# Kernel tuning notes

Measured on AMD Instinct MI355X. Metric: run time of the kernel, lower is better.

The kernel has to match this reference:

```python
import jax, jax.numpy as jnp
import numpy as np

N_HEADS = 16


def _rope_table(seq_len, head_dim):
    # Matches RotaryPositionalEmbedding: emb = cat(sin(pos*inv_freq), cos(pos*inv_freq))
    inv_freq = 1.0 / (10000.0 ** (jnp.arange(0, head_dim, 2, dtype=jnp.float32) / head_dim))
    sinusoid = jnp.arange(seq_len, dtype=jnp.float32)[:, None] * inv_freq[None, :]  # [S, hd/2]
    return jnp.sin(sinusoid), jnp.cos(sinusoid)


def _apply_rope(q, k, seq_len, head_dim):
    # Faithful to the torch code, which slices emb[:, :hd/2] (== sin) and calls it 'cos',
    # and emb[:, hd/2:] (== cos) and calls it 'sin'. We keep that exact math.
    sin_tab, cos_tab = _rope_table(seq_len, head_dim)
    c = sin_tab[None, None]  # named 'cos' in torch code, actually sin values
    s = cos_tab[None, None]  # named 'sin' in torch code, actually cos values
    half = head_dim // 2
    def rot(x):
        x1, x2 = x[..., :half], x[..., half:]
        return jnp.concatenate([x1 * c - x2 * s, x2 * c + x1 * s], axis=-1)
    return rot(q), rot(k)


def setup_inputs() -> dict:
    key = jax.random.key(0)
    ks = jax.random.split(key, 9)
    B, S, D = 4, 2048, 1024
    sc = 1.0 / np.sqrt(D)
    return {
        'hidden_states': jax.random.normal(ks[0], (B, S, D), jnp.float32),
        'Wq': jax.random.normal(ks[1], (D, D), jnp.float32) * sc,
        'bq': jax.random.normal(ks[2], (D,), jnp.float32) * 0.01,
        'Wk': jax.random.normal(ks[3], (D, D), jnp.float32) * sc,
        'bk': jax.random.normal(ks[4], (D,), jnp.float32) * 0.01,
        'Wv': jax.random.normal(ks[5], (D, D), jnp.float32) * sc,
        'bv': jax.random.normal(ks[6], (D,), jnp.float32) * 0.01,
        'Wo': jax.random.normal(ks[7], (D, D), jnp.float32) * sc,
        'bo': jax.random.normal(ks[8], (D,), jnp.float32) * 0.01,
    }


def reference(hidden_states, Wq, bq, Wk, bk, Wv, bv, Wo, bo):
    B, S, D = hidden_states.shape
    H = N_HEADS
    hd = D // H

    def proj(W, b):
        y = jnp.einsum('bsd,ed->bse', hidden_states, W) + b  # nn.Linear: x @ W.T + b
        return y.reshape(B, S, H, hd).transpose(0, 2, 1, 3)   # [B,H,S,hd]

    q = proj(Wq, bq)
    k = proj(Wk, bk)
    v = proj(Wv, bv)
    q, k = _apply_rope(q, k, S, hd)

    scale = 1.0 / np.sqrt(hd)
    scores = jnp.einsum('bhqd,bhkd->bhqk', q, k) * scale  # [B,H,S,S]
    attn = jax.nn.softmax(scores, axis=-1)
    ctx = jnp.einsum('bhqk,bhkd->bhqd', attn, v)          # [B,H,S,hd]
    ctx = ctx.transpose(0, 2, 1, 3).reshape(B, S, D)
    return jnp.einsum('bsd,ed->bse', ctx, Wo) + bo
```

## Files before the change

### kernel.cpp

```cpp
#include <hip/hip_runtime.h>
#include <math.h>

#define SEQ 2048
#define DMODEL 1024
#define NH 16
#define HD 64
#define BH 64
#define MROWS 8192
#define QKV_U16 8388608
#define LOG2E 1.4426950408889634f

typedef __attribute__((ext_vector_type(8))) _Float16 half8;
typedef __attribute__((ext_vector_type(4))) _Float16 half4;
typedef __attribute__((ext_vector_type(2))) __fp16 fp16v2;
typedef __attribute__((ext_vector_type(8))) short short8;
typedef __attribute__((ext_vector_type(4))) float floatx4;
typedef unsigned short ush;

union FH { _Float16 h; ush u; };
union PK { fp16v2 v; unsigned u; };
union PH { unsigned u[2]; half4 h; };

__device__ inline ush f2h(float x) { FH c; c.h = (_Float16)x; return c.u; }

__device__ inline void glds16(const ush* g, ush* l) {
  __builtin_amdgcn_global_load_lds((const __attribute__((address_space(1))) void*)g,
                                   (__attribute__((address_space(3))) void*)l, 16, 0, 0);
}

__global__ __launch_bounds__(256)
void cvt_kb(const float* __restrict__ src, ush* __restrict__ dst, int M) {
  __shared__ float T[64][33];
  const int t = threadIdx.x;
  const int k0 = blockIdx.x * 32, m0 = blockIdx.y * 64;
  {
    int row = t >> 2, c = (t & 3) * 8;
    const float* sp = src + (size_t)(m0 + row) * DMODEL + k0 + c;
    float4 x0 = *(const float4*)sp;
    float4 x1 = *(const float4*)(sp + 4);
    float xs[8] = {x0.x, x0.y, x0.z, x0.w, x1.x, x1.y, x1.z, x1.w};
#pragma unroll
    for (int j = 0; j < 8; ++j) T[row][c + j] = xs[j];
  }
  __syncthreads();
  const int ml = t & 63, kbl = t >> 6;
  short8 h8;
#pragma unroll
  for (int j = 0; j < 8; ++j) h8[j] = (short)f2h(T[ml][kbl * 8 + j]);
  *(short8*)(dst + ((size_t)(k0 / 8 + kbl) * M + m0 + ml) * 8) = h8;
}

__global__ __launch_bounds__(256)
void cvt_w4(const float* __restrict__ W0, const float* __restrict__ W1,
            const float* __restrict__ W2, const float* __restrict__ W3,
            ush* __restrict__ dst) {
  __shared__ float T[64][33];
  const int z = blockIdx.z;
  const float* src = (z == 0) ? W0 : (z == 1) ? W1 : (z == 2) ? W2 : W3;
  ush* dz = dst + (size_t)z * DMODEL * DMODEL;
  const int t = threadIdx.x;
  const int k0 = blockIdx.x * 32, m0 = blockIdx.y * 64;
  {
    int row = t >> 2, c = (t & 3) * 8;
    const float* sp = src + (size_t)(m0 + row) * DMODEL + k0 + c;
    float4 x0 = *(const float4*)sp;
    float4 x1 = *(const float4*)(sp + 4);
    float xs[8] = {x0.x, x0.y, x0.z, x0.w, x1.x, x1.y, x1.z, x1.w};
#pragma unroll
    for (int j = 0; j < 8; ++j) T[row][c + j] = xs[j];
  }
  __syncthreads();
  const int ml = t & 63, kbl = t >> 6;
  short8 h8;
#pragma unroll
  for (int j = 0; j < 8; ++j) h8[j] = (short)f2h(T[ml][kbl * 8 + j]);
  *(short8*)(dz + ((size_t)(k0 / 8 + kbl) * DMODEL + m0 + ml) * 8) = h8;
}

__global__ __launch_bounds__(256)
void sincos_kernel(float2* __restrict__ tab) {
  const int idx = blockIdx.x * 256 + threadIdx.x;
  const int s = idx >> 5, i = idx & 31;
  const float f = (float)pow(10000.0, -(double)i / 32.0);
  const float ang = (float)s * f;
  tab[idx] = make_float2(sinf(ang), cosf(ang));
}

template<int QKV>
__global__ __launch_bounds__(256, 4)
void gemm_f16(const ush* __restrict__ A, const ush* __restrict__ W0,
              const float* __restrict__ b0, const float* __restrict__ b1,
              const float* __restrict__ b2, void* __restrict__ out0,
              void* __restrict__ out1, void* __restrict__ out2,
              const float2* __restrict__ sctab) {
  __shared__ ush SA[2][4096];
  __shared__ ush SW[2][4096];
  const int tid  = threadIdx.x;
  const int wave = tid >> 6;
  const int lane = tid & 63;
  const int fr = lane & 15;
  const int fg = lane >> 4;
  const int wm = wave & 1;
  const int wn = wave >> 1;

  const int zz = QKV ? (blockIdx.x >> 3) : 3;
  const int nx = QKV ? (blockIdx.x & 7) : blockIdx.x;
  const int m0 = blockIdx.y * 128;
  const int n0 = nx * 128;
  const int m_base = m0 + wm * 64;
  const int n_base = n0 + wn * 64;

  const ush* W = W0 + (size_t)(QKV ? zz : 0) * (DMODEL * DMODEL);
  const float* bias = QKV ? (zz == 0 ? b0 : zz == 1 ? b1 : b2) : b0;
  void* outp = QKV ? (zz == 0 ? out0 : zz == 1 ? out1 : out2) : out0;
  const float scale = (QKV && zz == 0) ? 0.125f * LOG2E : 1.0f;

  floatx4 acc[4][4];
#pragma unroll
  for (int i = 0; i < 4; ++i)
#pragma unroll
    for (int j = 0; j < 4; ++j) acc[i][j] = (floatx4){0.f, 0.f, 0.f, 0.f};

  auto stage = [&](int b, int kb0) {
#pragma unroll
    for (int p = 0; p < 2; ++p) {
      const int eb = p * 256 + wave * 64;
      const int kb = eb >> 7, r0 = eb & 127;
      const ush* ga = A + (size_t)(kb0 + kb) * (MROWS * 8) + (size_t)(m0 + r0 + lane) * 8;
      glds16(ga, &SA[b][(size_t)eb * 8]);
      const ush* gw = W + (size_t)(kb0 + kb) * (DMODEL * 8) + (size_t)(n0 + r0 + lane) * 8;
      glds16(gw, &SW[b][(size_t)eb * 8]);
    }
  };

  auto compute = [&](int b) {
    const int kbl = fg;
    half8 ah[4], wh[4];
#pragma unroll
    for (int tm = 0; tm < 4; ++tm)
      ah[tm] = *(const half8*)&SA[b][(size_t)(kbl * 128 + wm * 64 + tm * 16 + fr) * 8];
#pragma unroll
    for (int tn = 0; tn < 4; ++tn)
      wh[tn] = *(const half8*)&SW[b][(size_t)(kbl * 128 + wn * 64 + tn * 16 + fr) * 8];
#pragma unroll
    for (int tm = 0; tm < 4; ++tm)
#pragma unroll
      for (int tn = 0; tn < 4; ++tn)
        acc[tm][tn] = __builtin_amdgcn_mfma_f32_16x16x32_f16(ah[tm], wh[tn], acc[tm][tn], 0, 0, 0);
  };

  stage(0, 0);
  __syncthreads();
  for (int t = 0; t < 32; ++t) {
    if (t + 1 < 32) stage((t + 1) & 1, (t + 1) * 4);
    compute(t & 1);
    __syncthreads();
  }

  float bias_s[4];
#pragma unroll
  for (int tn = 0; tn < 4; ++tn) bias_s[tn] = bias[n_base + tn * 16 + fr];

  if (!QKV) {
#pragma unroll
    for (int tm = 0; tm < 4; ++tm)
#pragma unroll
      for (int tn = 0; tn < 4; ++tn)
#pragma unroll
        for (int r = 0; r < 4; ++r) {
          const int m = m_base + tm * 16 + fg * 4 + r;
          const int n = n_base + tn * 16 + fr;
          ((float*)outp)[(size_t)m * DMODEL + n] = acc[tm][tn][r] + bias_s[tn];
        }
    return;
  }

  const int h = (n_base >> 6) & 15;
  ush* out = (ush*)outp;

  if (zz == 2) {
#pragma unroll
    for (int tm = 0; tm < 4; ++tm)
#pragma unroll
      for (int tn = 0; tn < 4; ++tn)
#pragma unroll
        for (int r = 0; r < 4; ++r) {
          const int m = m_base + tm * 16 + fg * 4 + r;
          const int s = m & (SEQ - 1);
          const size_t bh = (size_t)((m >> 11) * NH + h);
          const int d = tn * 16 + fr;
          const int k6 = s & 63, ktl = s >> 6;
          const int s2 = k6 >> 5;
          const int jj = ((k6 >> 4) & 1) * 4 + (k6 & 3);
          const int fgv = (k6 >> 2) & 3;
          const int dt = d >> 4, frv = d & 15;
          size_t pos = ((((bh * 32 + ktl) * 4 + dt) * 2 + s2) * 64 + fgv * 16 + frv) * 8 + jj;
          out[pos] = f2h(acc[tm][tn][r] + bias_s[tn]);
        }
    return;
  }

#pragma unroll
  for (int tn2 = 0; tn2 < 2; ++tn2) {
    const int i = tn2 * 16 + fr;
#pragma unroll
    for (int tm = 0; tm < 4; ++tm)
#pragma unroll
      for (int r = 0; r < 4; ++r) {
        const int m = m_base + tm * 16 + fg * 4 + r;
        const int s = m & (SEQ - 1);
        const size_t bh = (size_t)((m >> 11) * NH + h);
        const float x1 = acc[tm][tn2][r] + bias_s[tn2];
        const float x2 = acc[tm][tn2 + 2][r] + bias_s[tn2 + 2];
        const float2 sc = sctab[(s << 5) + i];
        const float sv = sc.x, cv = sc.y;
        const float o1 = (x1 * sv - x2 * cv) * scale;
        const float o2 = (x2 * sv + x1 * cv) * scale;
        const int d1 = i, d2 = i + 32;
#pragma unroll
        for (int e = 0; e < 2; ++e) {
          const int d = e ? d2 : d1;
          const float ov = e ? o2 : o1;
          const int ks = d >> 5, fgq = (d >> 3) & 3, j = d & 7;
          size_t pos;
          if (zz == 0) {
            const int qt = s >> 5, mm = (s >> 4) & 1, fr2 = s & 15;
            pos = ((((bh * 64 + qt) * 2 + mm) * 2 + ks) * 64 + fgq * 16 + fr2) * 8 + j;
          } else {
            const int ktl = s >> 6, jt = (s >> 4) & 3, fr2 = s & 15;
            pos = ((((bh * 32 + ktl) * 4 + jt) * 2 + ks) * 64 + fgq * 16 + fr2) * 8 + j;
          }
          out[pos] = f2h(ov);
        }
      }
  }
}

__global__ __launch_bounds__(256, 2)
void flash_mfma(const ush* __restrict__ qsw, const ush* __restrict__ ksw,
                const ush* __restrict__ vsw, ush* __restrict__ ctxf) {
  __shared__ __align__(16) ush Tep[4][64][72];
  __shared__ float Lden[4][64];
  const int tid = threadIdx.x;
  const int wave = tid >> 6;
  const int lane = tid & 63;
  const int fr = lane & 15;
  const int fg = lane >> 4;

  const int lin = blockIdx.x + 8 * blockIdx.y;
  const int xcd = lin & 7;
  const int t2  = lin >> 3;
  const int qblk = t2 & 7;
  const int bh   = xcd + 8 * (t2 >> 3);

  const int q0 = qblk * 256 + wave * 64;
  const ush* qp = qsw + ((size_t)bh * 64 + (q0 >> 5)) * 2048;
  const ush* kp = ksw + (size_t)bh * 131072;
  const ush* vp = vsw + (size_t)bh * 131072;

  half8 qf[4][2];
#pragma unroll
  for (int qn = 0; qn < 4; ++qn)
#pragma unroll
    for (int ks = 0; ks < 2; ++ks)
      qf[qn][ks] = *(const half8*)(qp + (qn * 2 + ks) * 512 + lane * 8);

  floatx4 oacc[4][4];
#pragma unroll
  for (int qn = 0; qn < 4; ++qn)
#pragma unroll
    for (int i = 0; i < 4; ++i) oacc[qn][i] = (floatx4){0.f, 0.f, 0.f, 0.f};
  float lsum[4] = {0.f, 0.f, 0.f, 0.f};

  const fp16v2 one2 = {(__fp16)1.0f, (__fp16)1.0f};

  for (int kt = 0; kt < 32; ++kt) {
    const ush* ktp = kp + kt * 4096;
    const ush* vtp = vp + kt * 4096;

    half8 kf[8], vf[8];
#pragma unroll
    for (int i = 0; i < 8; ++i) kf[i] = *(const half8*)(ktp + i * 512 + lane * 8);
#pragma unroll
    for (int i = 0; i < 8; ++i) vf[i] = *(const half8*)(vtp + i * 512 + lane * 8);

#pragma unroll
    for (int qn = 0; qn < 4; ++qn) {
      floatx4 s4[4];
#pragma unroll
      for (int jt = 0; jt < 4; ++jt) s4[jt] = (floatx4){0.f, 0.f, 0.f, 0.f};
#pragma unroll
      for (int ks = 0; ks < 2; ++ks)
#pragma unroll
        for (int jt = 0; jt < 4; ++jt)
          s4[jt] = __builtin_amdgcn_mfma_f32_16x16x32_f16(kf[jt * 2 + ks], qf[qn][ks], s4[jt], 0, 0, 0);

      half4 P[4];
#pragma unroll
      for (int jt = 0; jt < 4; ++jt) {
        float p0 = __builtin_amdgcn_exp2f(s4[jt][0]);
        float p1 = __builtin_amdgcn_exp2f(s4[jt][1]);
        float p2 = __builtin_amdgcn_exp2f(s4[jt][2]);
        float p3 = __builtin_amdgcn_exp2f(s4[jt][3]);
        PK a, b;
        a.v = __builtin_amdgcn_cvt_pkrtz(p0, p1);
        b.v = __builtin_amdgcn_cvt_pkrtz(p2, p3);
        lsum[qn] = __builtin_amdgcn_fdot2(a.v, one2, lsum[qn], false);
        lsum[qn] = __builtin_amdgcn_fdot2(b.v, one2, lsum[qn], false);
        PH ph; ph.u[0] = a.u; ph.u[1] = b.u;
        P[jt] = ph.h;
      }

#pragma unroll
      for (int sub = 0; sub < 4; ++sub) {
        const int s2 = sub >> 1, hk = sub & 1;
#pragma unroll
        for (int dt = 0; dt < 4; ++dt) {
          half8 v8 = vf[dt * 2 + s2];
          half4 vs = hk ? __builtin_shufflevector(v8, v8, 4, 5, 6, 7)
                        : __builtin_shufflevector(v8, v8, 0, 1, 2, 3);
          oacc[qn][dt] = __builtin_amdgcn_mfma_f32_16x16x16f16(P[sub], vs, oacc[qn][dt], 0, 0, 0);
        }
      }
    }
  }

#pragma unroll
  for (int qn = 0; qn < 4; ++qn) {
    lsum[qn] += __shfl_xor(lsum[qn], 16);
    lsum[qn] += __shfl_xor(lsum[qn], 32);
    Lden[wave][qn * 16 + fr] = lsum[qn];
  }

  const int b = bh >> 4, h = bh & 15;
#pragma unroll
  for (int qn = 0; qn < 4; ++qn)
#pragma unroll
    for (int r = 0; r < 4; ++r) {
      const float inv = 1.0f / Lden[wave][qn * 16 + fg * 4 + r];
#pragma unroll
      for (int dt = 0; dt < 4; ++dt)
        Tep[wave][qn * 16 + fg * 4 + r][dt * 16 + fr] = f2h(oacc[qn][dt][r] * inv);
    }
  const size_t mrow0 = (size_t)b * SEQ + q0;
  const int kb = lane >> 3;
#pragma unroll
  for (int i = 0; i < 8; ++i) {
    const int q = (lane & 7) + i * 8;
    short8 v = *(const short8*)&Tep[wave][q][kb * 8];
    *(short8*)(ctxf + ((size_t)(h * 8 + kb) * MROWS + mrow0 + q) * 8) = v;
  }
}

extern "C" void kernel_launch(void* const* d_in, const int* in_sizes, int n_in,
                              void* d_out, int out_size, void* d_ws, size_t ws_size,
                              hipStream_t stream) {
  const float* hs = (const float*)d_in[0];
  const float* Wq = (const float*)d_in[1];
  const float* bq = (const float*)d_in[2];
  const float* Wk = (const float*)d_in[3];
  const float* bk = (const float*)d_in[4];
  const float* Wv = (const float*)d_in[5];
  const float* bv = (const float*)d_in[6];
  const float* Wo = (const float*)d_in[7];
  const float* bo = (const float*)d_in[8];

  ush* qsw  = (ush*)d_ws;
  ush* ksw  = qsw + QKV_U16;
  ush* vsw  = ksw + QKV_U16;
  ush* hsf  = vsw + QKV_U16;
  ush* ctxf = hsf + QKV_U16;
  ush* Wf4  = ctxf + QKV_U16;
  float2* sctab = (float2*)(Wf4 + 4 * DMODEL * DMODEL);

  const size_t WS = (size_t)DMODEL * DMODEL;

  sincos_kernel<<<256, 256, 0, stream>>>(sctab);
  cvt_w4<<<dim3(32, 16, 4), 256, 0, stream>>>(Wq, Wk, Wv, Wo, Wf4);
  cvt_kb<<<dim3(32, 128), 256, 0, stream>>>(hs, hsf, MROWS);

  gemm_f16<1><<<dim3(24, 64), 256, 0, stream>>>(hsf, Wf4, bq, bk, bv,
                                                qsw, ksw, vsw, sctab);

  flash_mfma<<<dim3(8, BH), 256, 0, stream>>>(qsw, ksw, vsw, ctxf);

  gemm_f16<0><<<dim3(8, 64), 256, 0, stream>>>(ctxf, Wf4 + 3 * WS, bo, nullptr, nullptr,
                                               d_out, nullptr, nullptr, sctab);
}
```

Baseline: 300.0 us.

## Use 16x16x32 MFMA for PV, add setprio, narrow output GEMM tile

In the attention kernel, the PV product now uses the 16x16x32 f16 MFMA. It concatenates two P fragments into one half8, so it issues half as many instructions and no longer needs to shuffle V. The score and PV MFMA blocks are wrapped in s_setprio raises, so waves doing matrix work get issue priority over waves doing softmax. The output projection GEMM narrows its N tile from 128 to 64 and doubles the grid, so the 512 blocks become 1024 and fill more compute units. The cost is less reuse of A per block.

```diff
diff --git a/kernel.cpp b/kernel.cpp
--- a/kernel.cpp
+++ b/kernel.cpp
@@ -93,8 +93,10 @@
               const float* __restrict__ b2, void* __restrict__ out0,
               void* __restrict__ out1, void* __restrict__ out2,
               const float2* __restrict__ sctab) {
+  constexpr int BN = QKV ? 128 : 64;
+  constexpr int TN = QKV ? 4 : 2;
   __shared__ ush SA[2][4096];
-  __shared__ ush SW[2][4096];
+  __shared__ ush SW[2][BN * 32];
   const int tid  = threadIdx.x;
   const int wave = tid >> 6;
   const int lane = tid & 63;
@@ -106,20 +108,20 @@
   const int zz = QKV ? (blockIdx.x >> 3) : 3;
   const int nx = QKV ? (blockIdx.x & 7) : blockIdx.x;
   const int m0 = blockIdx.y * 128;
-  const int n0 = nx * 128;
+  const int n0 = nx * BN;
   const int m_base = m0 + wm * 64;
-  const int n_base = n0 + wn * 64;
+  const int n_base = n0 + wn * (TN * 16);
 
   const ush* W = W0 + (size_t)(QKV ? zz : 0) * (DMODEL * DMODEL);
   const float* bias = QKV ? (zz == 0 ? b0 : zz == 1 ? b1 : b2) : b0;
   void* outp = QKV ? (zz == 0 ? out0 : zz == 1 ? out1 : out2) : out0;
   const float scale = (QKV && zz == 0) ? 0.125f * LOG2E : 1.0f;
 
-  floatx4 acc[4][4];
+  floatx4 acc[4][TN];
 #pragma unroll
   for (int i = 0; i < 4; ++i)
 #pragma unroll
-    for (int j = 0; j < 4; ++j) acc[i][j] = (floatx4){0.f, 0.f, 0.f, 0.f};
+    for (int j = 0; j < TN; ++j) acc[i][j] = (floatx4){0.f, 0.f, 0.f, 0.f};
 
   auto stage = [&](int b, int kb0) {
 #pragma unroll
@@ -128,24 +130,34 @@
       const int kb = eb >> 7, r0 = eb & 127;
       const ush* ga = A + (size_t)(kb0 + kb) * (MROWS * 8) + (size_t)(m0 + r0 + lane) * 8;
       glds16(ga, &SA[b][(size_t)eb * 8]);
-      const ush* gw = W + (size_t)(kb0 + kb) * (DMODEL * 8) + (size_t)(n0 + r0 + lane) * 8;
-      glds16(gw, &SW[b][(size_t)eb * 8]);
+    }
+    if (QKV) {
+#pragma unroll
+      for (int p = 0; p < 2; ++p) {
+        const int eb = p * 256 + wave * 64;
+        const int kb = eb >> 7, r0 = eb & 127;
+        const ush* gw = W + (size_t)(kb0 + kb) * (DMODEL * 8) + (size_t)(n0 + r0 + lane) * 8;
+        glds16(gw, &SW[b][(size_t)eb * 8]);
+      }
+    } else {
+      const ush* gw = W + (size_t)(kb0 + wave) * (DMODEL * 8) + (size_t)(n0 + lane) * 8;
+      glds16(gw, &SW[b][(size_t)wave * 512]);
     }
   };
 
   auto compute = [&](int b) {
     const int kbl = fg;
-    half8 ah[4], wh[4];
+    half8 ah[4], wh[TN];
 #pragma unroll
     for (int tm = 0; tm < 4; ++tm)
       ah[tm] = *(const half8*)&SA[b][(size_t)(kbl * 128 + wm * 64 + tm * 16 + fr) * 8];
 #pragma unroll
-    for (int tn = 0; tn < 4; ++tn)
-      wh[tn] = *(const half8*)&SW[b][(size_t)(kbl * 128 + wn * 64 + tn * 16 + fr) * 8];
+    for (int tn = 0; tn < TN; ++tn)
+      wh[tn] = *(const half8*)&SW[b][(size_t)(kbl * BN + wn * (TN * 16) + tn * 16 + fr) * 8];
 #pragma unroll
     for (int tm = 0; tm < 4; ++tm)
 #pragma unroll
-      for (int tn = 0; tn < 4; ++tn)
+      for (int tn = 0; tn < TN; ++tn)
         acc[tm][tn] = __builtin_amdgcn_mfma_f32_16x16x32_f16(ah[tm], wh[tn], acc[tm][tn], 0, 0, 0);
   };
 
@@ -157,15 +169,15 @@
     __syncthreads();
   }
 
-  float bias_s[4];
-#pragma unroll
-  for (int tn = 0; tn < 4; ++tn) bias_s[tn] = bias[n_base + tn * 16 + fr];
+  float bias_s[TN];
+#pragma unroll
+  for (int tn = 0; tn < TN; ++tn) bias_s[tn] = bias[n_base + tn * 16 + fr];
 
   if (!QKV) {
 #pragma unroll
     for (int tm = 0; tm < 4; ++tm)
 #pragma unroll
-      for (int tn = 0; tn < 4; ++tn)
+      for (int tn = 0; tn < TN; ++tn)
 #pragma unroll
         for (int r = 0; r < 4; ++r) {
           const int m = m_base + tm * 16 + fg * 4 + r;
@@ -289,11 +301,13 @@
       floatx4 s4[4];
 #pragma unroll
       for (int jt = 0; jt < 4; ++jt) s4[jt] = (floatx4){0.f, 0.f, 0.f, 0.f};
+      __builtin_amdgcn_s_setprio(1);
 #pragma unroll
       for (int ks = 0; ks < 2; ++ks)
 #pragma unroll
         for (int jt = 0; jt < 4; ++jt)
           s4[jt] = __builtin_amdgcn_mfma_f32_16x16x32_f16(kf[jt * 2 + ks], qf[qn][ks], s4[jt], 0, 0, 0);
+      __builtin_amdgcn_s_setprio(0);
 
       half4 P[4];
 #pragma unroll
@@ -311,17 +325,15 @@
         P[jt] = ph.h;
       }
 
-#pragma unroll
-      for (int sub = 0; sub < 4; ++sub) {
-        const int s2 = sub >> 1, hk = sub & 1;
-#pragma unroll
-        for (int dt = 0; dt < 4; ++dt) {
-          half8 v8 = vf[dt * 2 + s2];
-          half4 vs = hk ? __builtin_shufflevector(v8, v8, 4, 5, 6, 7)
-                        : __builtin_shufflevector(v8, v8, 0, 1, 2, 3);
-          oacc[qn][dt] = __builtin_amdgcn_mfma_f32_16x16x16f16(P[sub], vs, oacc[qn][dt], 0, 0, 0);
-        }
+      __builtin_amdgcn_s_setprio(1);
+#pragma unroll
+      for (int s2 = 0; s2 < 2; ++s2) {
+        half8 p8 = __builtin_shufflevector(P[s2 * 2], P[s2 * 2 + 1], 0, 1, 2, 3, 4, 5, 6, 7);
+#pragma unroll
+        for (int dt = 0; dt < 4; ++dt)
+          oacc[qn][dt] = __builtin_amdgcn_mfma_f32_16x16x32_f16(p8, vf[dt * 2 + s2], oacc[qn][dt], 0, 0, 0);
       }
+      __builtin_amdgcn_s_setprio(0);
     }
   }
 
@@ -384,6 +396,6 @@
 
   flash_mfma<<<dim3(8, BH), 256, 0, stream>>>(qsw, ksw, vsw, ctxf);
 
-  gemm_f16<0><<<dim3(8, 64), 256, 0, stream>>>(ctxf, Wf4 + 3 * WS, bo, nullptr, nullptr,
-                                               d_out, nullptr, nullptr, sctab);
-}
+  gemm_f16<0><<<dim3(16, 64), 256, 0, stream>>>(ctxf, Wf4 + 3 * WS, bo, nullptr, nullptr,
+                                                d_out, nullptr, nullptr, sctab);
+}
```

Result: faster. 286.1 us (-4.6%).
